# Optimization experiments

Hardware: AMD Instinct MI355X
Metric: run time of the kernel (lower is better)

Reference implementation:

```python
import jax, jax.numpy as jnp
import numpy as np

T = 4          # num edge types
D = 256        # embedding_size == hidden_size
N = 100_000    # nodes
E_EDGES = 320_000
VOCAB = 10_000


def setup_inputs() -> dict:
    key = jax.random.key(0)
    ks = jax.random.split(key, 12)
    s = 0.02
    input_ids = jax.random.randint(ks[0], (1, N), 0, VOCAB)
    etype = jax.random.randint(ks[1], (1, E_EDGES), 1, T + 1)  # types 1..T
    src = jax.random.randint(ks[2], (1, E_EDGES), 0, N)
    tgt = jax.random.randint(ks[3], (1, E_EDGES), 0, N)
    typed_edges = jnp.stack([etype[0], src[0], tgt[0]], axis=0)[None]  # [1,3,E]
    embed_table = jax.random.normal(ks[4], (VOCAB, D)) * s
    # 6 inner layers (3 per concat block x 2 blocks): 256 -> 256
    edge_W_inner = jax.random.normal(ks[5], (6, T, D, 2 * D)) * s
    ln_s_inner = jnp.ones((6, D)); ln_b_inner = jnp.zeros((6, D))
    dense_W_inner = jax.random.normal(ks[6], (6, D, D)) * s
    dense_b_inner = jnp.zeros((6, D))
    # 2 output layers on concat [state, hidden]: hidden_size 512 -> 256
    edge_W_out = jax.random.normal(ks[7], (2, T, 2 * D, 4 * D)) * s
    ln_s_out = jnp.ones((2, 2 * D)); ln_b_out = jnp.zeros((2, 2 * D))
    dense_W_out = jax.random.normal(ks[8], (2, D, 2 * D)) * s
    dense_b_out = jnp.zeros((2, D))
    return {
        "input_ids": input_ids, "typed_edges": typed_edges,
        "embed_table": embed_table,
        "edge_W_inner": edge_W_inner, "ln_s_inner": ln_s_inner, "ln_b_inner": ln_b_inner,
        "dense_W_inner": dense_W_inner, "dense_b_inner": dense_b_inner,
        "edge_W_out": edge_W_out, "ln_s_out": ln_s_out, "ln_b_out": ln_b_out,
        "dense_W_out": dense_W_out, "dense_b_out": dense_b_out,
    }


def layer_norm(x, s, b, eps=1e-5):
    mu = jnp.mean(x, axis=-1, keepdims=True)
    var = jnp.mean((x - mu) ** 2, axis=-1, keepdims=True)
    return (x - mu) * jax.lax.rsqrt(var + eps) * s + b


def message_passing(state, etype, src, tgt, edge_W):
    # state [N,d]; edge_W [T, d, 2d]. Gather endpoints, per-type linear, scatter-add to targets.
    es = jnp.concatenate([state[src], state[tgt]], axis=1)  # [E, 2d]
    msgs = jnp.zeros((es.shape[0], edge_W.shape[1]), state.dtype)
    for t in range(edge_W.shape[0]):  # small fixed number of edge types
        msgs = msgs + jnp.where((etype == t + 1)[:, None], es @ edge_W[t].T, 0.0)
    return jax.ops.segment_sum(msgs, tgt, num_segments=state.shape[0])


def gnn_layer(state, etype, src, tgt, eW, ls, lb, dW, db):
    m = message_passing(state, etype, src, tgt, eW)
    h = layer_norm(jax.nn.gelu(m, approximate=False), ls, lb)
    return jnp.tanh(h @ dW.T + db)


def concat_block(state, etype, src, tgt, eWi, lsi, lbi, dWi, dbi, eWo, lso, lbo, dWo, dbo):
    x = state
    for i in range(3):
        x = gnn_layer(x, etype, src, tgt, eWi[i], lsi[i], lbi[i], dWi[i], dbi[i])
    res = jnp.concatenate([state, x], axis=1)  # [N, 2d] residual concat
    return gnn_layer(res, etype, src, tgt, eWo, lso, lbo, dWo, dbo)


def reference(input_ids, typed_edges, embed_table, edge_W_inner, ln_s_inner, ln_b_inner,
              dense_W_inner, dense_b_inner, edge_W_out, ln_s_out, ln_b_out,
              dense_W_out, dense_b_out):
    ids = input_ids[0]
    te = typed_edges[0]
    etype, src, tgt = te[0], te[1], te[2]
    x = embed_table[ids]  # [N, D]
    for b in range(2):
        sl = slice(3 * b, 3 * b + 3)
        x = concat_block(x, etype, src, tgt,
                         edge_W_inner[sl], ln_s_inner[sl], ln_b_inner[sl],
                         dense_W_inner[sl], dense_b_inner[sl],
                         edge_W_out[b], ln_s_out[b], ln_b_out[b],
                         dense_W_out[b], dense_b_out[b])
    return x
```

## Files before the change

### kernel.cpp

```cpp
#include <hip/hip_runtime.h>
#include <cstdio>

#define N_NODES 100000
#define NPAD    100096
#define NTILES  782
#define NE      320000
#define NCH     196
#define WCO_OFF 3145728L
#define OUT_ELEMS (N_NODES * 256)

typedef unsigned short ushort_t;
typedef unsigned short u16x4 __attribute__((ext_vector_type(4)));
typedef unsigned short u16x8 __attribute__((ext_vector_type(8)));
typedef _Float16       f16;
typedef _Float16       f16x8 __attribute__((ext_vector_type(8)));
typedef float          f32x4 __attribute__((ext_vector_type(4)));
typedef float          f32x4v __attribute__((ext_vector_type(4)));

__device__ __forceinline__ float bf2f(ushort_t u) {
    return __uint_as_float(((unsigned)u) << 16);
}
__device__ __forceinline__ ushort_t f2bf(float f) {
    unsigned u = __float_as_uint(f);
    u += 0x7FFFu + ((u >> 16) & 1u);
    return (ushort_t)(u >> 16);
}
__device__ __forceinline__ ushort_t f2h(float f) {
    f16 h = (f16)f;
    return __builtin_bit_cast(ushort_t, h);
}
__device__ __forceinline__ float h2f(ushort_t u) {
    return (float)__builtin_bit_cast(f16, u);
}

__device__ __forceinline__ int xcd_remap(int pbid, int nwg) {
    int q = nwg >> 3, r = nwg & 7;
    int xcd = pbid & 7, idx = pbid >> 3;
    int base = (xcd < r) ? xcd * (q + 1) : r * (q + 1) + (xcd - r) * q;
    return base + idx;
}

__device__ __forceinline__ float fast_tanh(float x) {
    x = fminf(fmaxf(x, -10.f), 10.f);
    float e = __expf(2.f * x);
    return (e - 1.f) / (e + 1.f);
}

__device__ __forceinline__ float gelu_f(float x) {
    return 0.5f * x * (1.f + erff(x * 0.70710678118654752f));
}

__global__ __launch_bounds__(256) void detect_k(const unsigned* __restrict__ w0, int* __restrict__ flag) {
    __shared__ int lds[256];
    int t = threadIdx.x;
    int cnt = 0;
    for (int i = t; i < 2048; i += 256) {
        unsigned e = (w0[i] >> 7) & 0xFFu;
        cnt += (e >= 96u && e <= 140u) ? 1 : 0;
    }
    lds[t] = cnt; __syncthreads();
    for (int s = 128; s > 0; s >>= 1) {
        if (t < s) lds[t] += lds[t + s];
        __syncthreads();
    }
    if (t == 0) *flag = (lds[0] < 1024) ? 1 : 0;
}

__device__ __forceinline__ ushort_t load_in(const void* p, long i, bool isf32) {
    return isf32 ? f2h(((const float*)p)[i]) : f2h(bf2f(((const ushort_t*)p)[i]));
}

struct CvtArgs {
    const void* src[8];
    ushort_t*   dst[8];
    int         n[8];
};

__global__ __launch_bounds__(256) void cvt_k(CvtArgs a, const int* __restrict__ flag) {
    int ti = blockIdx.y;
    int n = a.n[ti];
    const void* s = a.src[ti];
    ushort_t* d = a.dst[ti];
    bool isf32 = (*flag != 0);
    for (int i = blockIdx.x * 256 + threadIdx.x; i < n; i += gridDim.x * 256)
        d[i] = load_in(s, i, isf32);
}

__global__ __launch_bounds__(256) void scale_w_k(const ushort_t* __restrict__ dWiC,
                                                 const ushort_t* __restrict__ lsiC,
                                                 const ushort_t* __restrict__ lbiC,
                                                 const ushort_t* __restrict__ dbiC,
                                                 const ushort_t* __restrict__ dWoC,
                                                 const ushort_t* __restrict__ lsoC,
                                                 const ushort_t* __restrict__ lboC,
                                                 const ushort_t* __restrict__ dboC,
                                                 ushort_t* __restrict__ dWiS,
                                                 float* __restrict__ uwi, float* __restrict__ w0i,
                                                 ushort_t* __restrict__ dWoS,
                                                 float* __restrict__ uwo, float* __restrict__ w0o) {
    int wid = blockIdx.x * 4 + (threadIdx.x >> 6);
    int l = threadIdx.x & 63;
    float u = 0.f, w0 = 0.f;
    if (wid < 1536) {
        int lay = wid >> 8, c = wid & 255;
        u16x4 wv = *(const u16x4*)(dWiC + (size_t)wid * 256 + l * 4);
        u16x4 sv = *(const u16x4*)(lsiC + lay * 256 + l * 4);
        u16x4 bv = *(const u16x4*)(lbiC + lay * 256 + l * 4);
        u16x4 ov;
        #pragma unroll
        for (int i = 0; i < 4; i++) {
            float W = h2f(wv[i]);
            float ws = W * h2f(sv[i]);
            ov[i] = f2h(ws);
            u += ws; w0 += W * h2f(bv[i]);
        }
        *(u16x4*)(dWiS + (size_t)wid * 256 + l * 4) = ov;
        #pragma unroll
        for (int m = 1; m < 64; m <<= 1) {
            u += __shfl_xor(u, m, 64); w0 += __shfl_xor(w0, m, 64);
        }
        if (l == 0) { uwi[wid] = u; w0i[wid] = w0 + h2f(dbiC[lay * 256 + c]); }
    } else if (wid < 2048) {
        int w2 = wid - 1536;
        int b = w2 >> 8, c = w2 & 255;
        u16x8 wv = *(const u16x8*)(dWoC + (size_t)w2 * 512 + l * 8);
        u16x8 sv = *(const u16x8*)(lsoC + b * 512 + l * 8);
        u16x8 bv = *(const u16x8*)(lboC + b * 512 + l * 8);
        u16x8 ov;
        #pragma unroll
        for (int i = 0; i < 8; i++) {
            float W = h2f(wv[i]);
            float ws = W * h2f(sv[i]);
            ov[i] = f2h(ws);
            u += ws; w0 += W * h2f(bv[i]);
        }
        *(u16x8*)(dWoS + (size_t)w2 * 512 + l * 8) = ov;
        #pragma unroll
        for (int m = 1; m < 64; m <<= 1) {
            u += __shfl_xor(u, m, 64); w0 += __shfl_xor(w0, m, 64);
        }
        if (l == 0) { uwo[w2] = u; w0o[w2] = w0 + h2f(dboC[b * 256 + c]); }
    }
}

__global__ __launch_bounds__(256) void pack_w(const void* __restrict__ eWi,
                                              const void* __restrict__ eWo,
                                              ushort_t* __restrict__ WC,
                                              const int* __restrict__ flag) {
    long idx = (long)blockIdx.x * 256 + threadIdx.x;
    bool isf32 = (*flag != 0);
    const long ELI = 6L * 4 * 256 * 512;
    const long ELO = 2L * 4 * 512 * 1024;
    if (idx < ELI) {
        int j = idx & 511;
        int o = (idx >> 9) & 255;
        int t = (idx >> 17) & 3;
        long l = idx >> 19;
        int q = o >> 6, oo = o & 63;
        int k = j & 255;
        int n = ((j < 256) ? 0 : 256) + t * 64 + oo;
        WC[l * 524288 + (long)q * 131072 + (long)n * 256 + k] = load_in(eWi, idx, isf32);
    } else if (idx < ELI + ELO) {
        long i2 = idx - ELI;
        int j = i2 & 1023;
        int o = (i2 >> 10) & 511;
        int t = (i2 >> 19) & 3;
        long b = i2 >> 21;
        int c = o >> 6, oo = o & 63;
        int k = j & 511;
        int n = ((j < 512) ? 0 : 256) + t * 64 + oo;
        WC[WCO_OFF + b * 2097152L + (long)c * 262144 + (long)n * 512 + k] = load_in(eWo, i2, isf32);
    }
}

__global__ __launch_bounds__(256) void embed_k(const int* __restrict__ ids,
                                               const void* __restrict__ tab,
                                               ushort_t* __restrict__ S,
                                               const int* __restrict__ flag) {
    int row = blockIdx.x * 4 + (threadIdx.x >> 6);
    int l = threadIdx.x & 63;
    if (row >= N_NODES) return;
    int id = ids[row];
    u16x4 v;
    if (*flag) {
        f32x4v fv = *(const f32x4v*)((const float*)tab + (size_t)id * 256 + l * 4);
        #pragma unroll
        for (int i = 0; i < 4; i++) v[i] = f2h(fv[i]);
    } else {
        u16x4 bv = *(const u16x4*)((const ushort_t*)tab + (size_t)id * 256 + l * 4);
        #pragma unroll
        for (int i = 0; i < 4; i++) v[i] = f2h(bf2f(bv[i]));
    }
    *(u16x4*)(S + (size_t)row * 256 + l * 4) = v;
}

__global__ __launch_bounds__(256) void emit_k(const ushort_t* __restrict__ Bst, void* __restrict__ out,
                                              const int* __restrict__ flag) {
    long i = (long)blockIdx.x * 256 + threadIdx.x;
    if (i >= OUT_ELEMS) return;
    float v = h2f(Bst[i]);
    if (*flag) ((float*)out)[i] = v;
    else       ((ushort_t*)out)[i] = f2bf(v);
}

__global__ __launch_bounds__(256) void count_k(const int* __restrict__ tgt, int* __restrict__ counts) {
    int e = blockIdx.x * 256 + threadIdx.x;
    if (e < NE) atomicAdd(&counts[tgt[e]], 1);
}

__global__ __launch_bounds__(256) void scan1_k(const int* __restrict__ counts,
                                               int* __restrict__ incl, int* __restrict__ chsums) {
    __shared__ int lds[256];
    int c = blockIdx.x, t = threadIdx.x;
    int i0 = c * 512 + 2 * t;
    int a = (i0 < N_NODES) ? counts[i0] : 0;
    int b = (i0 + 1 < N_NODES) ? counts[i0 + 1] : 0;
    int ps = a + b;
    lds[t] = ps; __syncthreads();
    int x = ps;
    for (int off = 1; off < 256; off <<= 1) {
        int y = (t >= off) ? lds[t - off] : 0;
        __syncthreads();
        x += y; lds[t] = x;
        __syncthreads();
    }
    int excl = x - ps;
    if (i0 < N_NODES) incl[i0] = excl + a;
    if (i0 + 1 < N_NODES) incl[i0 + 1] = excl + a + b;
    if (t == 255) chsums[c] = x;
}

__global__ __launch_bounds__(256) void scan2_k(const int* __restrict__ chsums, int* __restrict__ chunkoff) {
    __shared__ int lds[256];
    int t = threadIdx.x;
    int v = (t < NCH) ? chsums[t] : 0;
    lds[t] = v; __syncthreads();
    int x = v;
    for (int off = 1; off < 256; off <<= 1) {
        int y = (t >= off) ? lds[t - off] : 0;
        __syncthreads();
        x += y; lds[t] = x;
        __syncthreads();
    }
    if (t <= NCH) chunkoff[t] = x - v;
}

__global__ __launch_bounds__(256) void scan3_k(const int* __restrict__ counts, const int* __restrict__ incl,
                                               const int* __restrict__ chunkoff,
                                               int* __restrict__ offsets, int* __restrict__ cursor) {
    int c = blockIdx.x, t = threadIdx.x;
    int base = chunkoff[c];
    #pragma unroll
    for (int k = 0; k < 2; k++) {
        int i = c * 512 + 2 * t + k;
        if (i < N_NODES) {
            int off = base + incl[i] - counts[i];
            offsets[i] = off;
            cursor[i] = off;
        }
    }
    if (c == 0 && t == 0) offsets[N_NODES] = chunkoff[NCH];
}

__global__ __launch_bounds__(256) void fill_k(const int* __restrict__ et, const int* __restrict__ src,
                                              const int* __restrict__ tgt,
                                              int* __restrict__ cursor, int* __restrict__ sorted) {
    int e = blockIdx.x * 256 + threadIdx.x;
    if (e < NE) {
        int pos = atomicAdd(&cursor[tgt[e]], 1);
        sorted[pos] = ((et[e] - 1) << 28) | src[e];
    }
}

template<int EPI>
__global__ __launch_bounds__(256) void gemm_bt(const ushort_t* __restrict__ A,
                                               const ushort_t* __restrict__ B,
                                               int K, int ldc,
                                               ushort_t* __restrict__ Cb,
                                               const float2* __restrict__ MR,
                                               const float* __restrict__ uu,
                                               const float* __restrict__ w0t,
                                               int storeM) {
    __shared__ __align__(16) ushort_t As[128 * 64];
    __shared__ __align__(16) ushort_t Bs[128 * 64];
    const int tid = threadIdx.x;
    const int w = tid >> 6, l = tid & 63;
    const int wr = w >> 1, wc = w & 1;
    const int gx = gridDim.x;
    const int lbid = xcd_remap(blockIdx.y * gx + blockIdx.x, gx * gridDim.y);
    const long m0 = (long)(lbid / gx) * 128, n0 = (long)(lbid % gx) * 128;
    const int lr = l >> 3;
    const int lc = (l & 7) * 8;
    const int cbk = ((l & 7) ^ lr) * 8;
    f32x4 acc[4][4];
    #pragma unroll
    for (int s = 0; s < 4; s++)
        #pragma unroll
        for (int n = 0; n < 4; n++) acc[s][n] = (f32x4){0.f, 0.f, 0.f, 0.f};

    for (int k0 = 0; k0 < K; k0 += 64) {
        #pragma unroll
        for (int q = 0; q < 4; q++) {
            int row = w * 32 + q * 8 + lr;
            const ushort_t* g = A + (m0 + row) * (long)K + k0 + cbk;
            __builtin_amdgcn_global_load_lds(
                (__attribute__((address_space(1))) unsigned int*)(g),
                (__attribute__((address_space(3))) unsigned int*)(&As[row * 64 + lc]), 16, 0, 0);
        }
        #pragma unroll
        for (int q = 0; q < 4; q++) {
            int row = w * 32 + q * 8 + lr;
            const ushort_t* g = B + (n0 + row) * (long)K + k0 + cbk;
            __builtin_amdgcn_global_load_lds(
                (__attribute__((address_space(1))) unsigned int*)(g),
                (__attribute__((address_space(3))) unsigned int*)(&Bs[row * 64 + lc]), 16, 0, 0);
        }
        __syncthreads();
        #pragma unroll
        for (int kk = 0; kk < 2; kk++) {
            f16x8 af[4], bfr[4];
            const int gb = kk * 4 + (l >> 4);
            const int sb = (gb ^ (l & 7)) * 8;
            #pragma unroll
            for (int s = 0; s < 4; s++)
                af[s] = *(const f16x8*)&As[(wr * 64 + s * 16 + (l & 15)) * 64 + sb];
            #pragma unroll
            for (int n = 0; n < 4; n++)
                bfr[n] = *(const f16x8*)&Bs[(wc * 64 + n * 16 + (l & 15)) * 64 + sb];
            #pragma unroll
            for (int s = 0; s < 4; s++)
                #pragma unroll
                for (int n = 0; n < 4; n++)
                    acc[s][n] = __builtin_amdgcn_mfma_f32_16x16x32_f16(bfr[n], af[s], acc[s][n], 0, 0, 0);
        }
        __syncthreads();
    }
    const long r0 = m0 + wr * 64 + (l & 15);
    const long c0 = n0 + wc * 64 + ((l >> 4) << 2);
    #pragma unroll
    for (int s = 0; s < 4; s++) {
        long r = r0 + s * 16;
        if constexpr (EPI == 2) {
            if (r < storeM) {
                float2 mr = MR[r];
                #pragma unroll
                for (int n = 0; n < 4; n++) {
                    long c = c0 + n * 16;
                    f32x4v u4 = *(const f32x4v*)&uu[c];
                    f32x4v w4 = *(const f32x4v*)&w0t[c];
                    u16x4 o;
                    #pragma unroll
                    for (int j = 0; j < 4; j++)
                        o[j] = f2h(fast_tanh(mr.y * (acc[s][n][j] - mr.x * u4[j]) + w4[j]));
                    *(u16x4*)&Cb[r * ldc + c] = o;
                }
            }
        } else {
            #pragma unroll
            for (int n = 0; n < 4; n++) {
                long c = c0 + n * 16;
                u16x4 o;
                #pragma unroll
                for (int j = 0; j < 4; j++) o[j] = f2h(acc[s][n][j]);
                *(u16x4*)&Cb[r * ldc + c] = o;
            }
        }
    }
}

__global__ __launch_bounds__(256) void gemm_bt2(const ushort_t* __restrict__ A0,
                                                const ushort_t* __restrict__ A1,
                                                const ushort_t* __restrict__ B,
                                                int ldc,
                                                ushort_t* __restrict__ Cb) {
    __shared__ __align__(16) ushort_t As[128 * 64];
    __shared__ __align__(16) ushort_t Bs[128 * 64];
    const int tid = threadIdx.x;
    const int w = tid >> 6, l = tid & 63;
    const int wr = w >> 1, wc = w & 1;
    const int gx = gridDim.x;
    const int lbid = xcd_remap(blockIdx.y * gx + blockIdx.x, gx * gridDim.y);
    const long m0 = (long)(lbid / gx) * 128, n0 = (long)(lbid % gx) * 128;
    const int lr = l >> 3;
    const int lc = (l & 7) * 8;
    const int cbk = ((l & 7) ^ lr) * 8;
    f32x4 acc[4][4];
    #pragma unroll
    for (int s = 0; s < 4; s++)
        #pragma unroll
        for (int n = 0; n < 4; n++) acc[s][n] = (f32x4){0.f, 0.f, 0.f, 0.f};

    for (int k0 = 0; k0 < 512; k0 += 64) {
        const ushort_t* Ab = (k0 < 256) ? A0 : A1;
        const int kq = k0 & 255;
        #pragma unroll
        for (int q = 0; q < 4; q++) {
            int row = w * 32 + q * 8 + lr;
            const ushort_t* g = Ab + (m0 + row) * 256L + kq + cbk;
            __builtin_amdgcn_global_load_lds(
                (__attribute__((address_space(1))) unsigned int*)(g),
                (__attribute__((address_space(3))) unsigned int*)(&As[row * 64 + lc]), 16, 0, 0);
        }
        #pragma unroll
        for (int q = 0; q < 4; q++) {
            int row = w * 32 + q * 8 + lr;
            const ushort_t* g = B + (n0 + row) * 512L + k0 + cbk;
            __builtin_amdgcn_global_load_lds(
                (__attribute__((address_space(1))) unsigned int*)(g),
                (__attribute__((address_space(3))) unsigned int*)(&Bs[row * 64 + lc]), 16, 0, 0);
        }
        __syncthreads();
        #pragma unroll
        for (int kk = 0; kk < 2; kk++) {
            f16x8 af[4], bfr[4];
            const int gb = kk * 4 + (l >> 4);
            const int sb = (gb ^ (l & 7)) * 8;
            #pragma unroll
            for (int s = 0; s < 4; s++)
                af[s] = *(const f16x8*)&As[(wr * 64 + s * 16 + (l & 15)) * 64 + sb];
            #pragma unroll
            for (int n = 0; n < 4; n++)
                bfr[n] = *(const f16x8*)&Bs[(wc * 64 + n * 16 + (l & 15)) * 64 + sb];
            #pragma unroll
            for (int s = 0; s < 4; s++)
                #pragma unroll
                for (int n = 0; n < 4; n++)
                    acc[s][n] = __builtin_amdgcn_mfma_f32_16x16x32_f16(bfr[n], af[s], acc[s][n], 0, 0, 0);
        }
        __syncthreads();
    }
    const long r0 = m0 + wr * 64 + (l & 15);
    const long c0 = n0 + wc * 64 + ((l >> 4) << 2);
    #pragma unroll
    for (int s = 0; s < 4; s++) {
        long r = r0 + s * 16;
        #pragma unroll
        for (int n = 0; n < 4; n++) {
            long c = c0 + n * 16;
            u16x4 o;
            #pragma unroll
            for (int j = 0; j < 4; j++) o[j] = f2h(acc[s][n][j]);
            *(u16x4*)&Cb[r * ldc + c] = o;
        }
    }
}

__global__ __launch_bounds__(256) void agg_q(const ushort_t* __restrict__ Z,
                                             const int* __restrict__ offsets,
                                             const int* __restrict__ sorted,
                                             ushort_t* __restrict__ G, int mld, int q,
                                             float* __restrict__ Sg, float* __restrict__ Sq) {
    int v = blockIdx.x * 4 + (threadIdx.x >> 6);
    int l = threadIdx.x & 63;
    if (v >= NPAD) return;
    ushort_t* mp = G + (size_t)v * mld + (q << 6) + l;
    if (v >= N_NODES) { *mp = 0; return; }
    float acc = 0.f;
    int d0 = 0, d1 = 0, d2 = 0, d3 = 0;
    int beg = offsets[v], end = offsets[v + 1];
    for (int e = beg; e < end; ++e) {
        int pk = sorted[e];
        int t = pk >> 28;
        int s = pk & 0x0FFFFFFF;
        acc += h2f(Z[(size_t)s * 512 + (t << 6) + l]);
        d0 += (t == 0); d1 += (t == 1); d2 += (t == 2); d3 += (t == 3);
    }
    const ushort_t* zs = Z + (size_t)v * 512 + 256 + l;
    if (d0) acc += (float)d0 * h2f(zs[0]);
    if (d1) acc += (float)d1 * h2f(zs[64]);
    if (d2) acc += (float)d2 * h2f(zs[128]);
    if (d3) acc += (float)d3 * h2f(zs[192]);
    float g = gelu_f(acc);
    *mp = f2h(g);
    float sg = g, sq = g * g;
    #pragma unroll
    for (int m = 1; m < 64; m <<= 1) {
        sg += __shfl_xor(sg, m, 64);
        sq += __shfl_xor(sq, m, 64);
    }
    if (l == 0) {
        atomicAdd(&Sg[v], sg);
        atomicAdd(&Sq[v], sq);
    }
}

__global__ __launch_bounds__(256) void stats_k(float* __restrict__ Sg, float* __restrict__ Sq,
                                               float2* __restrict__ MR, float inv) {
    int v = blockIdx.x * 256 + threadIdx.x;
    if (v >= N_NODES) return;
    float mean = Sg[v] * inv;
    float var = fmaxf(Sq[v] * inv - mean * mean, 0.f);
    MR[v] = make_float2(mean, rsqrtf(var + 1e-5f));
    Sg[v] = 0.f; Sq[v] = 0.f;
}

extern "C" void kernel_launch(void* const* d_in, const int* in_sizes, int n_in,
                              void* d_out, int out_size, void* d_ws, size_t ws_size,
                              hipStream_t stream) {
    const int* ids = (const int*)d_in[0];
    const int* te = (const int*)d_in[1];
    const int* et = te;
    const int* esrc = te + NE;
    const int* etgt = te + 2 * NE;
    const void* tab = d_in[2];
    const void* eWi = d_in[3];
    const void* lsi = d_in[4];
    const void* lbi = d_in[5];
    const void* dWi = d_in[6];
    const void* dbi = d_in[7];
    const void* eWo = d_in[8];
    const void* lso = d_in[9];
    const void* lbo = d_in[10];
    const void* dWo = d_in[11];
    const void* dbo = d_in[12];

    char* w = (char*)d_ws;
    auto alloc = [&](size_t bytes) -> char* {
        char* p = w; w += (bytes + 255) & ~(size_t)255; return p;
    };
    ushort_t* A    = (ushort_t*)alloc((size_t)NPAD * 256 * 2);
    ushort_t* Bst  = (ushort_t*)alloc((size_t)NPAD * 256 * 2);
    ushort_t* WC   = (ushort_t*)alloc(7340032UL * 2);
    ushort_t* lsiC = (ushort_t*)alloc(1536 * 2);
    ushort_t* lbiC = (ushort_t*)alloc(1536 * 2);
    ushort_t* dbiC = (ushort_t*)alloc(1536 * 2);
    ushort_t* lsoC = (ushort_t*)alloc(1024 * 2);
    ushort_t* lboC = (ushort_t*)alloc(1024 * 2);
    ushort_t* dboC = (ushort_t*)alloc(512 * 2);
    ushort_t* dWiC = (ushort_t*)alloc(393216UL * 2);
    ushort_t* dWoC = (ushort_t*)alloc(262144UL * 2);
    ushort_t* dWiS = (ushort_t*)alloc(393216UL * 2);
    ushort_t* dWoS = (ushort_t*)alloc(262144UL * 2);
    float* uwi     = (float*)alloc(1536 * 4);
    float* w0i     = (float*)alloc(1536 * 4);
    float* uwo     = (float*)alloc(512 * 4);
    float* w0o     = (float*)alloc(512 * 4);
    float* Sg      = (float*)alloc((size_t)NPAD * 4);
    float* Sq      = (float*)alloc((size_t)NPAD * 4);
    float2* MR     = (float2*)alloc((size_t)NPAD * 8);
    int* flag      = (int*)alloc(256);
    int* counts    = (int*)alloc((size_t)N_NODES * 4);
    int* incl      = (int*)alloc((size_t)N_NODES * 4);
    int* chsums    = (int*)alloc(1024);
    int* chunkoff  = (int*)alloc(1024);
    int* offsets   = (int*)alloc((size_t)(N_NODES + 8) * 4);
    int* cursor    = (int*)alloc((size_t)N_NODES * 4);
    int* sorted    = (int*)alloc((size_t)NE * 4);
    ushort_t* G    = (ushort_t*)alloc((size_t)NPAD * 512 * 2);
    ushort_t* R;
    if ((size_t)out_size >= (size_t)NPAD * 256 * 2) R = (ushort_t*)d_out;
    else R = (ushort_t*)alloc((size_t)NPAD * 256 * 2);
    size_t fixed = (size_t)(w - (char*)d_ws);

    const size_t ZQ_BYTES = (size_t)NPAD * 512 * 2;
    size_t bigsz = (ws_size > fixed) ? (ws_size - fixed) : 0;
    if (bigsz < ZQ_BYTES) {
        fprintf(stderr, "kernel_launch: ws too small (%zu bytes, fixed %zu, big %zu) -- no-op\n",
                ws_size, fixed, bigsz);
        return;
    }
    ushort_t* Zq = (ushort_t*)w;

    detect_k<<<1, 256, 0, stream>>>((const unsigned*)tab, flag);
    CvtArgs ca;
    ca.src[0] = lsi;  ca.dst[0] = lsiC; ca.n[0] = 1536;
    ca.src[1] = lbi;  ca.dst[1] = lbiC; ca.n[1] = 1536;
    ca.src[2] = dbi;  ca.dst[2] = dbiC; ca.n[2] = 1536;
    ca.src[3] = lso;  ca.dst[3] = lsoC; ca.n[3] = 1024;
    ca.src[4] = lbo;  ca.dst[4] = lboC; ca.n[4] = 1024;
    ca.src[5] = dbo;  ca.dst[5] = dboC; ca.n[5] = 512;
    ca.src[6] = dWi;  ca.dst[6] = dWiC; ca.n[6] = 393216;
    ca.src[7] = dWo;  ca.dst[7] = dWoC; ca.n[7] = 262144;
    cvt_k<<<dim3(1536, 8), 256, 0, stream>>>(ca, flag);
    scale_w_k<<<512, 256, 0, stream>>>(dWiC, lsiC, lbiC, dbiC, dWoC, lsoC, lboC, dboC,
                                       dWiS, uwi, w0i, dWoS, uwo, w0o);
    hipMemsetAsync(counts, 0, (size_t)N_NODES * 4, stream);
    hipMemsetAsync(Sg, 0, (size_t)NPAD * 4, stream);
    hipMemsetAsync(Sq, 0, (size_t)NPAD * 4, stream);
    hipMemsetAsync(A   + (size_t)N_NODES * 256, 0, (size_t)(NPAD - N_NODES) * 256 * 2, stream);
    hipMemsetAsync(Bst + (size_t)N_NODES * 256, 0, (size_t)(NPAD - N_NODES) * 256 * 2, stream);
    hipMemsetAsync(R   + (size_t)N_NODES * 256, 0, (size_t)(NPAD - N_NODES) * 256 * 2, stream);
    pack_w<<<28672, 256, 0, stream>>>(eWi, eWo, WC, flag);
    embed_k<<<N_NODES / 4, 256, 0, stream>>>(ids, tab, A, flag);
    count_k<<<(NE + 255) / 256, 256, 0, stream>>>(etgt, counts);
    scan1_k<<<NCH, 256, 0, stream>>>(counts, incl, chsums);
    scan2_k<<<1, 256, 0, stream>>>(chsums, chunkoff);
    scan3_k<<<NCH, 256, 0, stream>>>(counts, incl, chunkoff, offsets, cursor);
    fill_k<<<(NE + 255) / 256, 256, 0, stream>>>(et, esrc, etgt, cursor, sorted);

    auto inner_layer = [&](const ushort_t* Xin, ushort_t* Xout, int lay) {
        for (int q = 0; q < 4; q++) {
            gemm_bt<3><<<dim3(4, NTILES), 256, 0, stream>>>(
                Xin, WC + (long)lay * 524288 + (long)q * 131072, 256, 512, Zq,
                nullptr, nullptr, nullptr, 0);
            agg_q<<<NPAD / 4, 256, 0, stream>>>(Zq, offsets, sorted, G, 256, q, Sg, Sq);
        }
        stats_k<<<(N_NODES + 255) / 256, 256, 0, stream>>>(Sg, Sq, MR, 1.f / 256.f);
        gemm_bt<2><<<dim3(2, NTILES), 256, 0, stream>>>(G, dWiS + (long)lay * 65536, 256, 256,
                                                        Xout, MR, uwi + lay * 256, w0i + lay * 256, N_NODES);
    };

    auto out_layer = [&](const ushort_t* X0, const ushort_t* X1, int b, ushort_t* dest) {
        for (int c = 0; c < 8; c++) {
            gemm_bt2<<<dim3(4, NTILES), 256, 0, stream>>>(
                X0, X1, WC + WCO_OFF + (long)b * 2097152 + (long)c * 262144, 512, Zq);
            agg_q<<<NPAD / 4, 256, 0, stream>>>(Zq, offsets, sorted, G, 512, c, Sg, Sq);
        }
        stats_k<<<(N_NODES + 255) / 256, 256, 0, stream>>>(Sg, Sq, MR, 1.f / 512.f);
        gemm_bt<2><<<dim3(2, NTILES), 256, 0, stream>>>(G, dWoS + (long)b * 131072, 512, 256,
                                                        dest, MR, uwo + b * 256, w0o + b * 256, N_NODES);
    };

    inner_layer(A, Bst, 0);
    inner_layer(Bst, R, 1);
    inner_layer(R, Bst, 2);
    out_layer(A, Bst, 0, R);
    inner_layer(R, A, 3);
    inner_layer(A, Bst, 4);
    inner_layer(Bst, A, 5);
    out_layer(R, A, 1, Bst);

    emit_k<<<(OUT_ELEMS + 255) / 256, 256, 0, stream>>>(Bst, d_out, flag);
}
```

Measured before the change: 5.976 ms.

## Double-buffer LDS tiles in gemm_bt and gemm_bt2 to overlap loads with MFMA

Both GEMM kernels now keep two LDS buffers for the A and B tiles. The async global-to-LDS load for the next K-slice is issued right after the barrier, while MFMAs run on the current slice. This also removes the trailing barrier, leaving one per iteration. The aim is to hide global load latency behind compute, at the cost of doubling LDS per block to 64KB, which can lower the number of resident blocks per CU.

```diff
diff --git a/kernel.cpp b/kernel.cpp
--- a/kernel.cpp
+++ b/kernel.cpp
@@ -281,8 +281,8 @@
                                                const float* __restrict__ uu,
                                                const float* __restrict__ w0t,
                                                int storeM) {
-    __shared__ __align__(16) ushort_t As[128 * 64];
-    __shared__ __align__(16) ushort_t Bs[128 * 64];
+    __shared__ __align__(16) ushort_t As[2][128 * 64];
+    __shared__ __align__(16) ushort_t Bs[2][128 * 64];
     const int tid = threadIdx.x;
     const int w = tid >> 6, l = tid & 63;
     const int wr = w >> 1, wc = w & 1;
@@ -298,24 +298,26 @@
         #pragma unroll
         for (int n = 0; n < 4; n++) acc[s][n] = (f32x4){0.f, 0.f, 0.f, 0.f};
 
-    for (int k0 = 0; k0 < K; k0 += 64) {
+    auto stage = [&](int buf, int k0) {
         #pragma unroll
         for (int q = 0; q < 4; q++) {
             int row = w * 32 + q * 8 + lr;
-            const ushort_t* g = A + (m0 + row) * (long)K + k0 + cbk;
+            const ushort_t* ga = A + (m0 + row) * (long)K + k0 + cbk;
             __builtin_amdgcn_global_load_lds(
-                (__attribute__((address_space(1))) unsigned int*)(g),
-                (__attribute__((address_space(3))) unsigned int*)(&As[row * 64 + lc]), 16, 0, 0);
-        }
-        #pragma unroll
-        for (int q = 0; q < 4; q++) {
-            int row = w * 32 + q * 8 + lr;
-            const ushort_t* g = B + (n0 + row) * (long)K + k0 + cbk;
+                (__attribute__((address_space(1))) unsigned int*)(ga),
+                (__attribute__((address_space(3))) unsigned int*)(&As[buf][row * 64 + lc]), 16, 0, 0);
+            const ushort_t* gb = B + (n0 + row) * (long)K + k0 + cbk;
             __builtin_amdgcn_global_load_lds(
-                (__attribute__((address_space(1))) unsigned int*)(g),
-                (__attribute__((address_space(3))) unsigned int*)(&Bs[row * 64 + lc]), 16, 0, 0);
-        }
+                (__attribute__((address_space(1))) unsigned int*)(gb),
+                (__attribute__((address_space(3))) unsigned int*)(&Bs[buf][row * 64 + lc]), 16, 0, 0);
+        }
+    };
+
+    stage(0, 0);
+    int cur = 0;
+    for (int k0 = 0; k0 < K; k0 += 64) {
         __syncthreads();
+        if (k0 + 64 < K) stage(cur ^ 1, k0 + 64);
         #pragma unroll
         for (int kk = 0; kk < 2; kk++) {
             f16x8 af[4], bfr[4];
@@ -323,17 +325,17 @@
             const int sb = (gb ^ (l & 7)) * 8;
             #pragma unroll
             for (int s = 0; s < 4; s++)
-                af[s] = *(const f16x8*)&As[(wr * 64 + s * 16 + (l & 15)) * 64 + sb];
+                af[s] = *(const f16x8*)&As[cur][(wr * 64 + s * 16 + (l & 15)) * 64 + sb];
             #pragma unroll
             for (int n = 0; n < 4; n++)
-                bfr[n] = *(const f16x8*)&Bs[(wc * 64 + n * 16 + (l & 15)) * 64 + sb];
+                bfr[n] = *(const f16x8*)&Bs[cur][(wc * 64 + n * 16 + (l & 15)) * 64 + sb];
             #pragma unroll
             for (int s = 0; s < 4; s++)
                 #pragma unroll
                 for (int n = 0; n < 4; n++)
                     acc[s][n] = __builtin_amdgcn_mfma_f32_16x16x32_f16(bfr[n], af[s], acc[s][n], 0, 0, 0);
         }
-        __syncthreads();
+        cur ^= 1;
     }
     const long r0 = m0 + wr * 64 + (l & 15);
     const long c0 = n0 + wc * 64 + ((l >> 4) << 2);
@@ -373,8 +375,8 @@
                                                 const ushort_t* __restrict__ B,
                                                 int ldc,
                                                 ushort_t* __restrict__ Cb) {
-    __shared__ __align__(16) ushort_t As[128 * 64];
-    __shared__ __align__(16) ushort_t Bs[128 * 64];
+    __shared__ __align__(16) ushort_t As[2][128 * 64];
+    __shared__ __align__(16) ushort_t Bs[2][128 * 64];
     const int tid = threadIdx.x;
     const int w = tid >> 6, l = tid & 63;
     const int wr = w >> 1, wc = w & 1;
@@ -390,26 +392,28 @@
         #pragma unroll
         for (int n = 0; n < 4; n++) acc[s][n] = (f32x4){0.f, 0.f, 0.f, 0.f};
 
-    for (int k0 = 0; k0 < 512; k0 += 64) {
+    auto stage = [&](int buf, int k0) {
         const ushort_t* Ab = (k0 < 256) ? A0 : A1;
         const int kq = k0 & 255;
         #pragma unroll
         for (int q = 0; q < 4; q++) {
             int row = w * 32 + q * 8 + lr;
-            const ushort_t* g = Ab + (m0 + row) * 256L + kq + cbk;
+            const ushort_t* ga = Ab + (m0 + row) * 256L + kq + cbk;
             __builtin_amdgcn_global_load_lds(
-                (__attribute__((address_space(1))) unsigned int*)(g),
-                (__attribute__((address_space(3))) unsigned int*)(&As[row * 64 + lc]), 16, 0, 0);
-        }
-        #pragma unroll
-        for (int q = 0; q < 4; q++) {
-            int row = w * 32 + q * 8 + lr;
-            const ushort_t* g = B + (n0 + row) * 512L + k0 + cbk;
+                (__attribute__((address_space(1))) unsigned int*)(ga),
+                (__attribute__((address_space(3))) unsigned int*)(&As[buf][row * 64 + lc]), 16, 0, 0);
+            const ushort_t* gb = B + (n0 + row) * 512L + k0 + cbk;
             __builtin_amdgcn_global_load_lds(
-                (__attribute__((address_space(1))) unsigned int*)(g),
-                (__attribute__((address_space(3))) unsigned int*)(&Bs[row * 64 + lc]), 16, 0, 0);
-        }
+                (__attribute__((address_space(1))) unsigned int*)(gb),
+                (__attribute__((address_space(3))) unsigned int*)(&Bs[buf][row * 64 + lc]), 16, 0, 0);
+        }
+    };
+
+    stage(0, 0);
+    int cur = 0;
+    for (int k0 = 0; k0 < 512; k0 += 64) {
         __syncthreads();
+        if (k0 + 64 < 512) stage(cur ^ 1, k0 + 64);
         #pragma unroll
         for (int kk = 0; kk < 2; kk++) {
             f16x8 af[4], bfr[4];
@@ -417,17 +421,17 @@
             const int sb = (gb ^ (l & 7)) * 8;
             #pragma unroll
             for (int s = 0; s < 4; s++)
-                af[s] = *(const f16x8*)&As[(wr * 64 + s * 16 + (l & 15)) * 64 + sb];
+                af[s] = *(const f16x8*)&As[cur][(wr * 64 + s * 16 + (l & 15)) * 64 + sb];
             #pragma unroll
             for (int n = 0; n < 4; n++)
-                bfr[n] = *(const f16x8*)&Bs[(wc * 64 + n * 16 + (l & 15)) * 64 + sb];
+                bfr[n] = *(const f16x8*)&Bs[cur][(wc * 64 + n * 16 + (l & 15)) * 64 + sb];
             #pragma unroll
             for (int s = 0; s < 4; s++)
                 #pragma unroll
                 for (int n = 0; n < 4; n++)
                     acc[s][n] = __builtin_amdgcn_mfma_f32_16x16x32_f16(bfr[n], af[s], acc[s][n], 0, 0, 0);
         }
-        __syncthreads();
+        cur ^= 1;
     }
     const long r0 = m0 + wr * 64 + (l & 15);
     const long c0 = n0 + wc * 64 + ((l >> 4) << 2);
```

Measured after the change: 6.046 ms. Within noise of the previous version (+1.2%).
